# Optimization experiments

Hardware: AMD Instinct MI355X
Metric: run time of the kernel (lower is better)

The kernel has to match this reference:

```python
import jax, jax.numpy as jnp
import numpy as np

EPS = 1e-07


def setup_inputs() -> dict:
    key = jax.random.key(0)
    ks = jax.random.split(key, 5)
    B, Cin, Cout, H, W, K, S = 8, 512, 512, 64, 64, 3, 512
    return {
        "x": jax.random.normal(ks[0], (B, Cin, H, W), dtype=jnp.float32),
        "style": jax.random.normal(ks[1], (B, S), dtype=jnp.float32),
        "weight": jax.random.normal(ks[2], (1, Cout, Cin, K, K), dtype=jnp.float32),
        "mod_w": jax.random.normal(ks[3], (Cin, S), dtype=jnp.float32) * (1.0 / np.sqrt(S)),
        "mod_b": jax.random.normal(ks[4], (Cin,), dtype=jnp.float32) * 0.01,
    }


def reference(x, style, weight, mod_w, mod_b):
    B, Cin, H, W = x.shape
    Cout, K = weight.shape[1], weight.shape[3]
    scale = 1.0 / np.sqrt(Cin * K * K)
    # modulation: plain linear (EqualLinear.forward never applies self.scale)
    s = (style @ mod_w.T + mod_b).reshape(B, 1, Cin, 1, 1)
    w = scale * weight * s  # [B, Cout, Cin, K, K]
    demod = jax.lax.rsqrt(jnp.sum(w * w, axis=(2, 3, 4), keepdims=True) + EPS)
    # NOTE: source divides by rsqrt (i.e. multiplies by sqrt) -- kept faithful
    w = w / demod
    w = w.reshape(B * Cout, Cin, K, K)
    xr = x.reshape(1, B * Cin, H, W)
    pad = (K - 1) // 2
    out = jax.lax.conv_general_dilated(
        xr, w,
        window_strides=(1, 1),
        padding=((pad, pad), (pad, pad)),
        dimension_numbers=("NCHW", "OIHW", "NCHW"),
        feature_group_count=B,
    )
    return out.reshape(B, Cout, H, W)
```

## Files before the change

kernel.cpp:

```cpp
#include <hip/hip_runtime.h>
#include <hip/hip_bf16.h>
#include <stdint.h>
#include <math.h>

#define EPSV 1e-7f
#define B_   8
#define CIN  512
#define COUT 512
#define HH   64
#define WW   64
#define SS   512
#define HP   66
#define WP   66
#define NP   (HH*WW)

typedef __attribute__((ext_vector_type(8)))  short bf16x8;
typedef __attribute__((ext_vector_type(4)))  float f32x4;

#define MODSCALE 0.014731391274719739f

__global__ __launch_bounds__(256) void k_mod(const float* __restrict__ style,
                                             const float* __restrict__ mod_w,
                                             const float* __restrict__ mod_b,
                                             float* __restrict__ m_out) {
    int tid = threadIdx.x;
    int id = blockIdx.x * 64 + (tid >> 2);
    int b = id >> 9, ci = id & 511, q = tid & 3;
    const float4* st = (const float4*)(style + (size_t)b * SS);
    const float4* mw = (const float4*)(mod_w + (size_t)ci * SS);
    float acc = 0.f;
    #pragma unroll
    for (int j = 0; j < 32; ++j) {
        float4 s4 = st[q * 32 + j];
        float4 w4 = mw[q * 32 + j];
        acc += s4.x * w4.x + s4.y * w4.y + s4.z * w4.z + s4.w * w4.w;
    }
    acc += __shfl_xor(acc, 1);
    acc += __shfl_xor(acc, 2);
    if (q == 0) m_out[id] = MODSCALE * (acc + mod_b[ci]);
}

__global__ __launch_bounds__(256) void k_wprep(const float* __restrict__ weight,
                                               const float* __restrict__ m_buf,
                                               __hip_bfloat16* __restrict__ wt,
                                               float* __restrict__ dfac) {
    const int co  = blockIdx.x;
    const int tid = threadIdx.x;
    const int lane = tid & 63, wid = tid >> 6;
    __shared__ float wrow[4608];
    __shared__ float red[4][8];
    const float2* wsrc = (const float2*)(weight + (size_t)co * 4608);
    #pragma unroll
    for (int i = 0; i < 9; ++i)
        *(float2*)&wrow[(i * 256 + tid) * 2] = wsrc[i * 256 + tid];
    __syncthreads();
    float w0[9], w1[9], sq0 = 0.f, sq1 = 0.f;
    #pragma unroll
    for (int t = 0; t < 9; ++t) {
        w0[t] = wrow[tid * 9 + t];
        w1[t] = wrow[(tid + 256) * 9 + t];
        sq0 += w0[t] * w0[t];
        sq1 += w1[t] * w1[t];
    }
    float part[8];
    #pragma unroll
    for (int b = 0; b < 8; ++b) {
        float m0 = m_buf[b * CIN + tid];
        float m1 = m_buf[b * CIN + tid + 256];
        part[b] = sq0 * m0 * m0 + sq1 * m1 * m1;
    }
    #pragma unroll
    for (int b = 0; b < 8; ++b) {
        float v = part[b];
        #pragma unroll
        for (int off = 32; off > 0; off >>= 1) v += __shfl_xor(v, off);
        part[b] = v;
    }
    if (lane == 0) {
        #pragma unroll
        for (int b = 0; b < 8; ++b) red[wid][b] = part[b];
    }
    #pragma unroll
    for (int t = 0; t < 9; ++t) {
        size_t base = (size_t)t * COUT * CIN + (size_t)co * CIN;
        wt[base + tid]       = __float2bfloat16(w0[t]);
        wt[base + tid + 256] = __float2bfloat16(w1[t]);
    }
    __syncthreads();
    if (tid < 8)
        dfac[tid * COUT + co] =
            sqrtf(red[0][tid] + red[1][tid] + red[2][tid] + red[3][tid] + EPSV);
}

__global__ __launch_bounds__(256) void k_xpad(const float* __restrict__ x,
                                              const float* __restrict__ m_buf,
                                              __hip_bfloat16* __restrict__ xpad) {
    const int b = blockIdx.x >> 6;
    const int h = blockIdx.x & 63;
    const int tid = threadIdx.x;
    __shared__ float tile[64][65];
    for (int ci0 = 0; ci0 < CIN; ci0 += 64) {
        #pragma unroll
        for (int it = 0; it < 4; ++it) {
            int idx = it * 256 + tid;
            int w4 = idx & 15, cil = idx >> 4;
            float4 v = *(const float4*)&x[(((size_t)b * CIN + ci0 + cil) * HH + h) * WW + 4 * w4];
            tile[cil][4 * w4 + 0] = v.x; tile[cil][4 * w4 + 1] = v.y;
            tile[cil][4 * w4 + 2] = v.z; tile[cil][4 * w4 + 3] = v.w;
        }
        __syncthreads();
        #pragma unroll
        for (int it = 0; it < 4; ++it) {
            int idx = it * 256 + tid;
            int c4 = idx & 15, w = idx >> 4;
            float4 mv = *(const float4*)&m_buf[b * CIN + ci0 + 4 * c4];
            __hip_bfloat16 t0 = __float2bfloat16(tile[4 * c4 + 0][w] * mv.x);
            __hip_bfloat16 t1 = __float2bfloat16(tile[4 * c4 + 1][w] * mv.y);
            __hip_bfloat16 t2 = __float2bfloat16(tile[4 * c4 + 2][w] * mv.z);
            __hip_bfloat16 t3 = __float2bfloat16(tile[4 * c4 + 3][w] * mv.w);
            ushort4 pk = make_ushort4(*(unsigned short*)&t0, *(unsigned short*)&t1,
                                      *(unsigned short*)&t2, *(unsigned short*)&t3);
            *(ushort4*)&xpad[(((size_t)b * HP + h + 1) * WP + (w + 1)) * CIN + ci0 + 4 * c4] = pk;
        }
        __syncthreads();
    }
    const size_t base = (size_t)b * HP * WP * CIN;
    const ushort4 z4 = make_ushort4(0, 0, 0, 0);
    {
        int wp = (tid < 128) ? 0 : 65;
        int e  = (tid & 127) * 4;
        *(ushort4*)&xpad[base + ((size_t)(h + 1) * WP + wp) * CIN + e] = z4;
    }
    if (h == 0 || h == 63) {
        int hp = (h == 0) ? 0 : 65;
        for (int i = tid; i < (HP * CIN) / 4; i += 256)
            *(ushort4*)&xpad[base + (size_t)hp * WP * CIN + (size_t)i * 4] = z4;
    }
}


#define MM(A,B,C) __builtin_amdgcn_mfma_f32_16x16x32_bf16(A,B,C,0,0,0)

#define GLDS(GP, LOFF) __builtin_amdgcn_global_load_lds( \
    (const __attribute__((address_space(1))) void*)(GP), \
    (__attribute__((address_space(3))) void*)(smem + (LOFF)), 16, 0, 0)

#define LDA(SB, M) (*(const bf16x8*)(aLds + ((SB)*16384 + (M)*1024)))
#define LDB(SB, N) (*(const bf16x8*)(bLds + ((SB)*16384 + (N)*1024)))

#define STAGE_A(KT, SB) { const int t3_ = (KT) >> 4, ci3_ = ((KT) & 15) * 32;   \
    const size_t aB_ = (size_t)t3_ * (COUT * CIN) + ci3_;                       \
    GLDS(wt + aB_ + gA0, (SB) * 16384 + ldsd);                                  \
    GLDS(wt + aB_ + gA1, (SB) * 16384 + 8192 + ldsd); }

#define STAGE_B(KT, SB) { const int t3_ = (KT) >> 4, ci3_ = ((KT) & 15) * 32;   \
    const int bO_ = ((t3_ / 3) * WP + (t3_ % 3)) * CIN + ci3_;                  \
    GLDS(xpad + bO_ + gB0, 65536 + (SB) * 16384 + ldsd);                        \
    GLDS(xpad + bO_ + gB1, 65536 + (SB) * 16384 + 8192 + ldsd); }

#define BARRIER asm volatile("s_barrier" ::: "memory")
#define VM8 asm volatile("s_waitcnt vmcnt(8)" ::: "memory");
#define VM4 asm volatile("s_waitcnt vmcnt(4)" ::: "memory");
#define VM0 asm volatile("s_waitcnt vmcnt(0)" ::: "memory");
#define VMNONE

#define CCOL(N, BV) acc[0][N]=MM(ca0,BV,acc[0][N]); acc[1][N]=MM(ca1,BV,acc[1][N]); \
                    acc[2][N]=MM(ca2,BV,acc[2][N]); acc[3][N]=MM(ca3,BV,acc[3][N]);
#define XCOL(N, BV) acc[4][N]=MM(x4_,BV,acc[4][N]); acc[5][N]=MM(x5_,BV,acc[5][N]); \
                    acc[6][N]=MM(x6_,BV,acc[6][N]); acc[7][N]=MM(x7_,BV,acc[7][N]);

#define KTILE3(KK, SB, DOSTAGE, WAITER, DONEXT) {                               \
    cb2 = LDB(SB, 2); cb3 = LDB(SB, 3);                                         \
    bf16x8 x4_ = LDA(SB,4), x5_ = LDA(SB,5), x6_ = LDA(SB,6), x7_ = LDA(SB,7);  \
    if (DOSTAGE) { STAGE_A((KK)+3, ((SB)+3)&3); STAGE_B((KK)+3, ((SB)+3)&3); }  \
    __builtin_amdgcn_s_setprio(1);                                              \
    CCOL(0, cb0) CCOL(1, cb1) CCOL(2, cb2) CCOL(3, cb3)                         \
    __builtin_amdgcn_s_setprio(0);                                              \
    __builtin_amdgcn_sched_barrier(0);                                          \
    WAITER                                                                      \
    BARRIER;                                                                    \
    __builtin_amdgcn_sched_barrier(0);                                          \
    if (DONEXT) { const int nsb_ = ((SB)+1)&3;                                  \
        ca0 = LDA(nsb_,0); ca1 = LDA(nsb_,1);                                   \
        ca2 = LDA(nsb_,2); ca3 = LDA(nsb_,3);                                   \
        nb0_ = LDB(nsb_,0); nb1_ = LDB(nsb_,1);                                 \
    }                                                                           \
    __builtin_amdgcn_s_setprio(1);                                              \
    XCOL(0, cb0) XCOL(1, cb1) XCOL(2, cb2) XCOL(3, cb3)                         \
    __builtin_amdgcn_s_setprio(0);                                              \
    cb0 = nb0_; cb1 = nb1_;                                                     \
}

__global__ __launch_bounds__(512, 2) void k_conv(const __hip_bfloat16* __restrict__ wt,
                                                 const __hip_bfloat16* __restrict__ xpad,
                                                 const float* __restrict__ dfac,
                                                 float* __restrict__ out) {
    __shared__ __align__(16) char smem[131072];

    const int tid  = threadIdx.x;
    const int lane = tid & 63;
    const int wid  = tid >> 6;
    const int wr   = wid >> 2;
    const int wc   = wid & 3;
    const int frow = lane & 15;
    const int fk   = lane >> 4;

    const int bid = blockIdx.x;
    const int bb  = bid & 7;
    const int pt  = (bid >> 3) & 15;
    const int ct  = bid >> 7;
    const int co0 = ct * 256;
    const int p0  = pt * 256;

    const int xr = (fk ^ ((frow >> 1) & 3)) * 16;
    const char* aLds = smem + (wr * 8192 + frow * 64 + xr);
    const char* bLds = smem + 65536 + (wc * 4096 + frow * 64 + xr);

    const int ldsd = wid * 1024 + lane * 16;
    const int srow = wid * 16 + (lane >> 2);
    const int cg   = ((lane & 3) ^ ((lane >> 3) & 3)) * 8;
    const int gA0  = (co0 + srow) * CIN + cg;
    const int gA1  = (co0 + 128 + srow) * CIN + cg;
    const int pp0  = p0 + srow;
    const int pp1  = p0 + 128 + srow;
    const int gB0  = ((bb * HP + (pp0 >> 6)) * WP + (pp0 & 63)) * CIN + cg;
    const int gB1  = ((bb * HP + (pp1 >> 6)) * WP + (pp1 & 63)) * CIN + cg;

    f32x4 acc[8][4];
    #pragma unroll
    for (int m = 0; m < 8; ++m)
        #pragma unroll
        for (int n = 0; n < 4; ++n)
            acc[m][n] = (f32x4){0.f, 0.f, 0.f, 0.f};

    bf16x8 ca0, ca1, ca2, ca3, cb0, cb1, cb2, cb3, nb0_, nb1_;

    STAGE_A(0, 0) STAGE_B(0, 0)
    STAGE_A(1, 1) STAGE_B(1, 1)
    STAGE_A(2, 2) STAGE_B(2, 2)
    VM8;
    BARRIER;
    ca0 = LDA(0, 0); ca1 = LDA(0, 1); ca2 = LDA(0, 2); ca3 = LDA(0, 3);
    cb0 = LDB(0, 0); cb1 = LDB(0, 1);

    for (int k4 = 0; k4 < 140; k4 += 4) {
        KTILE3(k4 + 0, 0, 1, VM8, 1)
        KTILE3(k4 + 1, 1, 1, VM8, 1)
        KTILE3(k4 + 2, 2, 1, VM8, 1)
        KTILE3(k4 + 3, 3, 1, VM8, 1)
    }
    KTILE3(140, 0, 1, VM8, 1)
    KTILE3(141, 1, 0, VM4, 1)
    KTILE3(142, 2, 0, VM0, 1)
    KTILE3(143, 3, 0, VMNONE, 0)

    const float* dfb = dfac + bb * COUT;
    #pragma unroll
    for (int m = 0; m < 8; ++m) {
        int co = co0 + wr * 128 + m * 16 + fk * 4;
        float d0 = dfb[co + 0], d1 = dfb[co + 1], d2 = dfb[co + 2], d3 = dfb[co + 3];
        #pragma unroll
        for (int n = 0; n < 4; ++n) {
            int p = p0 + wc * 64 + n * 16 + frow;
            size_t ob = ((size_t)(bb * COUT + co)) * NP + p;
            out[ob]          = acc[m][n][0] * d0;
            out[ob + NP]     = acc[m][n][1] * d1;
            out[ob + 2 * NP] = acc[m][n][2] * d2;
            out[ob + 3 * NP] = acc[m][n][3] * d3;
        }
    }
}

extern "C" void kernel_launch(void* const* d_in, const int* in_sizes, int n_in,
                              void* d_out, int out_size, void* d_ws, size_t ws_size,
                              hipStream_t stream) {
    const float* x      = (const float*)d_in[0];
    const float* style  = (const float*)d_in[1];
    const float* weight = (const float*)d_in[2];
    const float* mod_w  = (const float*)d_in[3];
    const float* mod_b  = (const float*)d_in[4];
    float* out = (float*)d_out;

    char* ws = (char*)d_ws;
    const size_t M_OFF    = 0;
    const size_t DFAC_OFF = 16384;
    const size_t WT_OFF   = 32768;
    const size_t XPAD_OFF = WT_OFF + (size_t)9 * COUT * CIN * 2;

    float*          m_buf = (float*)(ws + M_OFF);
    float*          dfac  = (float*)(ws + DFAC_OFF);
    __hip_bfloat16* wt    = (__hip_bfloat16*)(ws + WT_OFF);
    __hip_bfloat16* xpad  = (__hip_bfloat16*)(ws + XPAD_OFF);

    k_mod<<<64, 256, 0, stream>>>(style, mod_w, mod_b, m_buf);
    k_wprep<<<512, 256, 0, stream>>>(weight, m_buf, wt, dfac);
    k_xpad<<<B_ * HH, 256, 0, stream>>>(x, m_buf, xpad);

    k_conv<<<256, 512, 0, stream>>>(wt, xpad, dfac, out);
}
```

Baseline: 158.2 us.

## Load weight operand directly from global into registers, bypassing LDS staging

```diff
diff --git a/kernel.cpp b/kernel.cpp
--- a/kernel.cpp
+++ b/kernel.cpp
@@ -145,44 +145,39 @@
     (const __attribute__((address_space(1))) void*)(GP), \
     (__attribute__((address_space(3))) void*)(smem + (LOFF)), 16, 0, 0)
 
-#define LDA(SB, M) (*(const bf16x8*)(aLds + ((SB)*16384 + (M)*1024)))
 #define LDB(SB, N) (*(const bf16x8*)(bLds + ((SB)*16384 + (N)*1024)))
 
-#define STAGE_A(KT, SB) { const int t3_ = (KT) >> 4, ci3_ = ((KT) & 15) * 32;   \
-    const size_t aB_ = (size_t)t3_ * (COUT * CIN) + ci3_;                       \
-    GLDS(wt + aB_ + gA0, (SB) * 16384 + ldsd);                                  \
-    GLDS(wt + aB_ + gA1, (SB) * 16384 + 8192 + ldsd); }
+#define AG(KT, M) (*(const bf16x8*)(wt + (size_t)((KT) >> 4) * (COUT * CIN) \
+                                    + (((KT) & 15) * 32) + aBase + (M) * (16 * CIN)))
 
 #define STAGE_B(KT, SB) { const int t3_ = (KT) >> 4, ci3_ = ((KT) & 15) * 32;   \
     const int bO_ = ((t3_ / 3) * WP + (t3_ % 3)) * CIN + ci3_;                  \
-    GLDS(xpad + bO_ + gB0, 65536 + (SB) * 16384 + ldsd);                        \
-    GLDS(xpad + bO_ + gB1, 65536 + (SB) * 16384 + 8192 + ldsd); }
+    GLDS(xpad + bO_ + gB0, (SB) * 16384 + ldsd);                                \
+    GLDS(xpad + bO_ + gB1, (SB) * 16384 + 8192 + ldsd); }
 
 #define BARRIER asm volatile("s_barrier" ::: "memory")
-#define VM8 asm volatile("s_waitcnt vmcnt(8)" ::: "memory");
+#define VM6 asm volatile("s_waitcnt vmcnt(6)" ::: "memory");
 #define VM4 asm volatile("s_waitcnt vmcnt(4)" ::: "memory");
-#define VM0 asm volatile("s_waitcnt vmcnt(0)" ::: "memory");
-#define VMNONE
 
 #define CCOL(N, BV) acc[0][N]=MM(ca0,BV,acc[0][N]); acc[1][N]=MM(ca1,BV,acc[1][N]); \
                     acc[2][N]=MM(ca2,BV,acc[2][N]); acc[3][N]=MM(ca3,BV,acc[3][N]);
 #define XCOL(N, BV) acc[4][N]=MM(x4_,BV,acc[4][N]); acc[5][N]=MM(x5_,BV,acc[5][N]); \
                     acc[6][N]=MM(x6_,BV,acc[6][N]); acc[7][N]=MM(x7_,BV,acc[7][N]);
 
-#define KTILE3(KK, SB, DOSTAGE, WAITER, DONEXT) {                               \
+#define KTILE4(KK, SB, DOSTAGE, DONEXT) {                                       \
     cb2 = LDB(SB, 2); cb3 = LDB(SB, 3);                                         \
-    bf16x8 x4_ = LDA(SB,4), x5_ = LDA(SB,5), x6_ = LDA(SB,6), x7_ = LDA(SB,7);  \
-    if (DOSTAGE) { STAGE_A((KK)+3, ((SB)+3)&3); STAGE_B((KK)+3, ((SB)+3)&3); }  \
+    bf16x8 x4_ = AG(KK,4), x5_ = AG(KK,5), x6_ = AG(KK,6), x7_ = AG(KK,7);      \
+    if (DOSTAGE) { STAGE_B((KK)+3, ((SB)+3)&3); }                               \
     __builtin_amdgcn_s_setprio(1);                                              \
     CCOL(0, cb0) CCOL(1, cb1) CCOL(2, cb2) CCOL(3, cb3)                         \
     __builtin_amdgcn_s_setprio(0);                                              \
     __builtin_amdgcn_sched_barrier(0);                                          \
-    WAITER                                                                      \
+    VM6                                                                         \
     BARRIER;                                                                    \
     __builtin_amdgcn_sched_barrier(0);                                          \
     if (DONEXT) { const int nsb_ = ((SB)+1)&3;                                  \
-        ca0 = LDA(nsb_,0); ca1 = LDA(nsb_,1);                                   \
-        ca2 = LDA(nsb_,2); ca3 = LDA(nsb_,3);                                   \
+        ca0 = AG((KK)+1,0); ca1 = AG((KK)+1,1);                                 \
+        ca2 = AG((KK)+1,2); ca3 = AG((KK)+1,3);                                 \
         nb0_ = LDB(nsb_,0); nb1_ = LDB(nsb_,1);                                 \
     }                                                                           \
     __builtin_amdgcn_s_setprio(1);                                              \
@@ -195,7 +190,7 @@
                                                  const __hip_bfloat16* __restrict__ xpad,
                                                  const float* __restrict__ dfac,
                                                  float* __restrict__ out) {
-    __shared__ __align__(16) char smem[131072];
+    __shared__ __align__(16) char smem[65536];
 
     const int tid  = threadIdx.x;
     const int lane = tid & 63;
@@ -213,14 +208,13 @@
     const int p0  = pt * 256;
 
     const int xr = (fk ^ ((frow >> 1) & 3)) * 16;
-    const char* aLds = smem + (wr * 8192 + frow * 64 + xr);
-    const char* bLds = smem + 65536 + (wc * 4096 + frow * 64 + xr);
-
-    const int ldsd = wid * 1024 + lane * 16;
+    const char* bLds = smem + (wc * 4096 + frow * 64 + xr);
+
+    const int aBase = (co0 + wr * 128 + frow) * CIN + fk * 8;
+
+    const int ldsd = tid * 16;
     const int srow = wid * 16 + (lane >> 2);
     const int cg   = ((lane & 3) ^ ((lane >> 3) & 3)) * 8;
-    const int gA0  = (co0 + srow) * CIN + cg;
-    const int gA1  = (co0 + 128 + srow) * CIN + cg;
     const int pp0  = p0 + srow;
     const int pp1  = p0 + 128 + srow;
     const int gB0  = ((bb * HP + (pp0 >> 6)) * WP + (pp0 & 63)) * CIN + cg;
@@ -235,24 +229,24 @@
 
     bf16x8 ca0, ca1, ca2, ca3, cb0, cb1, cb2, cb3, nb0_, nb1_;
 
-    STAGE_A(0, 0) STAGE_B(0, 0)
-    STAGE_A(1, 1) STAGE_B(1, 1)
-    STAGE_A(2, 2) STAGE_B(2, 2)
-    VM8;
+    STAGE_B(0, 0)
+    STAGE_B(1, 1)
+    STAGE_B(2, 2)
+    VM4;
     BARRIER;
-    ca0 = LDA(0, 0); ca1 = LDA(0, 1); ca2 = LDA(0, 2); ca3 = LDA(0, 3);
     cb0 = LDB(0, 0); cb1 = LDB(0, 1);
+    ca0 = AG(0, 0); ca1 = AG(0, 1); ca2 = AG(0, 2); ca3 = AG(0, 3);
 
     for (int k4 = 0; k4 < 140; k4 += 4) {
-        KTILE3(k4 + 0, 0, 1, VM8, 1)
-        KTILE3(k4 + 1, 1, 1, VM8, 1)
-        KTILE3(k4 + 2, 2, 1, VM8, 1)
-        KTILE3(k4 + 3, 3, 1, VM8, 1)
-    }
-    KTILE3(140, 0, 1, VM8, 1)
-    KTILE3(141, 1, 0, VM4, 1)
-    KTILE3(142, 2, 0, VM0, 1)
-    KTILE3(143, 3, 0, VMNONE, 0)
+        KTILE4(k4 + 0, 0, 1, 1)
+        KTILE4(k4 + 1, 1, 1, 1)
+        KTILE4(k4 + 2, 2, 1, 1)
+        KTILE4(k4 + 3, 3, 1, 1)
+    }
+    KTILE4(140, 0, 1, 1)
+    KTILE4(141, 1, 0, 1)
+    KTILE4(142, 2, 0, 1)
+    KTILE4(143, 3, 0, 0)
 
     const float* dfb = dfac + bb * COUT;
     #pragma unroll
```

New measurement: 357.7 us. 126% more time.

## Split xpad prep across channel quarters and prefetch all B fragments early

Applied to the files above, without the earlier changes.

```diff
diff --git a/kernel.cpp b/kernel.cpp
--- a/kernel.cpp
+++ b/kernel.cpp
@@ -95,46 +95,52 @@
 __global__ __launch_bounds__(256) void k_xpad(const float* __restrict__ x,
                                               const float* __restrict__ m_buf,
                                               __hip_bfloat16* __restrict__ xpad) {
-    const int b = blockIdx.x >> 6;
-    const int h = blockIdx.x & 63;
+    const int bidx = blockIdx.x;
+    const int q = bidx & 3;
+    const int h = (bidx >> 2) & 63;
+    const int b = bidx >> 8;
     const int tid = threadIdx.x;
-    __shared__ float tile[64][65];
-    for (int ci0 = 0; ci0 < CIN; ci0 += 64) {
-        #pragma unroll
-        for (int it = 0; it < 4; ++it) {
-            int idx = it * 256 + tid;
-            int w4 = idx & 15, cil = idx >> 4;
-            float4 v = *(const float4*)&x[(((size_t)b * CIN + ci0 + cil) * HH + h) * WW + 4 * w4];
-            tile[cil][4 * w4 + 0] = v.x; tile[cil][4 * w4 + 1] = v.y;
-            tile[cil][4 * w4 + 2] = v.z; tile[cil][4 * w4 + 3] = v.w;
+    const int ci0 = q * 128;
+    __shared__ float tile[128][65];
+
+    #pragma unroll
+    for (int it = 0; it < 8; ++it) {
+        int idx = it * 256 + tid;
+        int w4 = idx & 15, cl = idx >> 4;
+        float4 v = *(const float4*)&x[(((size_t)b * CIN + ci0 + cl) * HH + h) * WW + 4 * w4];
+        float* dst = &tile[cl][4 * (w4 ^ (cl >> 3))];
+        dst[0] = v.x; dst[1] = v.y; dst[2] = v.z; dst[3] = v.w;
+    }
+    __syncthreads();
+
+    #pragma unroll
+    for (int it = 0; it < 4; ++it) {
+        int idx = it * 256 + tid;
+        int cg = idx & 15, w = idx >> 4;
+        int pcol = 4 * ((w >> 2) ^ cg) + (w & 3);
+        bf16x8 pk;
+        #pragma unroll
+        for (int j = 0; j < 8; ++j) {
+            float mv = m_buf[b * CIN + ci0 + 8 * cg + j];
+            __hip_bfloat16 t = __float2bfloat16(tile[8 * cg + j][pcol] * mv);
+            pk[j] = *(short*)&t;
         }
-        __syncthreads();
-        #pragma unroll
-        for (int it = 0; it < 4; ++it) {
-            int idx = it * 256 + tid;
-            int c4 = idx & 15, w = idx >> 4;
-            float4 mv = *(const float4*)&m_buf[b * CIN + ci0 + 4 * c4];
-            __hip_bfloat16 t0 = __float2bfloat16(tile[4 * c4 + 0][w] * mv.x);
-            __hip_bfloat16 t1 = __float2bfloat16(tile[4 * c4 + 1][w] * mv.y);
-            __hip_bfloat16 t2 = __float2bfloat16(tile[4 * c4 + 2][w] * mv.z);
-            __hip_bfloat16 t3 = __float2bfloat16(tile[4 * c4 + 3][w] * mv.w);
-            ushort4 pk = make_ushort4(*(unsigned short*)&t0, *(unsigned short*)&t1,
-                                      *(unsigned short*)&t2, *(unsigned short*)&t3);
-            *(ushort4*)&xpad[(((size_t)b * HP + h + 1) * WP + (w + 1)) * CIN + ci0 + 4 * c4] = pk;
-        }
-        __syncthreads();
-    }
+        *(bf16x8*)&xpad[(((size_t)b * HP + h + 1) * WP + (w + 1)) * CIN + ci0 + 8 * cg] = pk;
+    }
+
     const size_t base = (size_t)b * HP * WP * CIN;
-    const ushort4 z4 = make_ushort4(0, 0, 0, 0);
-    {
-        int wp = (tid < 128) ? 0 : 65;
-        int e  = (tid & 127) * 4;
-        *(ushort4*)&xpad[base + ((size_t)(h + 1) * WP + wp) * CIN + e] = z4;
+    const bf16x8 z8 = (bf16x8)(short)0;
+    if (tid < 32) {
+        int wp = (tid >> 4) ? 65 : 0;
+        int grp = tid & 15;
+        *(bf16x8*)&xpad[base + ((size_t)(h + 1) * WP + wp) * CIN + ci0 + 8 * grp] = z8;
     }
     if (h == 0 || h == 63) {
         int hp = (h == 0) ? 0 : 65;
-        for (int i = tid; i < (HP * CIN) / 4; i += 256)
-            *(ushort4*)&xpad[base + (size_t)hp * WP * CIN + (size_t)i * 4] = z4;
+        for (int i = tid; i < 66 * 16; i += 256) {
+            int wp = i >> 4, grp = i & 15;
+            *(bf16x8*)&xpad[base + ((size_t)hp * WP + wp) * CIN + ci0 + 8 * grp] = z8;
+        }
     }
 }
 
@@ -170,7 +176,6 @@
                     acc[6][N]=MM(x6_,BV,acc[6][N]); acc[7][N]=MM(x7_,BV,acc[7][N]);
 
 #define KTILE3(KK, SB, DOSTAGE, WAITER, DONEXT) {                               \
-    cb2 = LDB(SB, 2); cb3 = LDB(SB, 3);                                         \
     bf16x8 x4_ = LDA(SB,4), x5_ = LDA(SB,5), x6_ = LDA(SB,6), x7_ = LDA(SB,7);  \
     if (DOSTAGE) { STAGE_A((KK)+3, ((SB)+3)&3); STAGE_B((KK)+3, ((SB)+3)&3); }  \
     __builtin_amdgcn_s_setprio(1);                                              \
@@ -184,11 +189,12 @@
         ca0 = LDA(nsb_,0); ca1 = LDA(nsb_,1);                                   \
         ca2 = LDA(nsb_,2); ca3 = LDA(nsb_,3);                                   \
         nb0_ = LDB(nsb_,0); nb1_ = LDB(nsb_,1);                                 \
+        nb2_ = LDB(nsb_,2); nb3_ = LDB(nsb_,3);                                 \
     }                                                                           \
     __builtin_amdgcn_s_setprio(1);                                              \
     XCOL(0, cb0) XCOL(1, cb1) XCOL(2, cb2) XCOL(3, cb3)                         \
     __builtin_amdgcn_s_setprio(0);                                              \
-    cb0 = nb0_; cb1 = nb1_;                                                     \
+    cb0 = nb0_; cb1 = nb1_; cb2 = nb2_; cb3 = nb3_;                             \
 }
 
 __global__ __launch_bounds__(512, 2) void k_conv(const __hip_bfloat16* __restrict__ wt,
@@ -233,7 +239,7 @@
         for (int n = 0; n < 4; ++n)
             acc[m][n] = (f32x4){0.f, 0.f, 0.f, 0.f};
 
-    bf16x8 ca0, ca1, ca2, ca3, cb0, cb1, cb2, cb3, nb0_, nb1_;
+    bf16x8 ca0, ca1, ca2, ca3, cb0, cb1, cb2, cb3, nb0_, nb1_, nb2_, nb3_;
 
     STAGE_A(0, 0) STAGE_B(0, 0)
     STAGE_A(1, 1) STAGE_B(1, 1)
@@ -241,7 +247,7 @@
     VM8;
     BARRIER;
     ca0 = LDA(0, 0); ca1 = LDA(0, 1); ca2 = LDA(0, 2); ca3 = LDA(0, 3);
-    cb0 = LDB(0, 0); cb1 = LDB(0, 1);
+    cb0 = LDB(0, 0); cb1 = LDB(0, 1); cb2 = LDB(0, 2); cb3 = LDB(0, 3);
 
     for (int k4 = 0; k4 < 140; k4 += 4) {
         KTILE3(k4 + 0, 0, 1, VM8, 1)
@@ -294,7 +300,7 @@
 
     k_mod<<<64, 256, 0, stream>>>(style, mod_w, mod_b, m_buf);
     k_wprep<<<512, 256, 0, stream>>>(weight, m_buf, wt, dfac);
-    k_xpad<<<B_ * HH, 256, 0, stream>>>(x, m_buf, xpad);
+    k_xpad<<<2048, 256, 0, stream>>>(x, m_buf, xpad);
 
     k_conv<<<256, 512, 0, stream>>>(wt, xpad, dfac, out);
 }
```

Measured after the change: 153.4 us. 3.0% less time.
